# Kernel optimization log

Measured on AMD Instinct MI355X. Metric: run time of the kernel, lower is better.

The kernel has to match this reference:

```python
import jax, jax.numpy as jnp
import numpy as np


def silu(x):
    return x * jax.nn.sigmoid(x)


def conv1x1(x, w, s, b, act):
    # x: [B,Ci,H,W], w: [Co,Ci]; BN folded into per-channel scale s / bias b
    y = jnp.einsum('oi,bihw->bohw', w, x) * s[None, :, None, None] + b[None, :, None, None]
    return silu(y) if act else y


def dwconv3x3(x, w, s, b):
    # depthwise 3x3, groups=C, padding SAME (autopad=1); w: [C,1,3,3]
    y = jax.lax.conv_general_dilated(
        x, w, window_strides=(1, 1), padding=[(1, 1), (1, 1)],
        dimension_numbers=('NCHW', 'OIHW', 'NCHW'),
        feature_group_count=x.shape[1])
    return y * s[None, :, None, None] + b[None, :, None, None]


def attention(x, qkv_w, qkv_s, qkv_b, pe_w, pe_s, pe_b, proj_w, proj_s, proj_b,
              num_heads=4, key_dim=32, head_dim=64):
    B, C, H, W = x.shape
    N = H * W
    scale = key_dim ** -0.5
    qkv = conv1x1(x, qkv_w, qkv_s, qkv_b, act=False)          # [B, C+2*nh*kd, H, W]
    qkv = qkv.reshape(B, num_heads, key_dim * 2 + head_dim, N)
    q = qkv[:, :, :key_dim]                                    # [B,nh,kd,N]
    k = qkv[:, :, key_dim:2 * key_dim]                         # [B,nh,kd,N]
    v = qkv[:, :, 2 * key_dim:]                                # [B,nh,hd,N]
    attn = jnp.einsum('bhdi,bhdj->bhij', q, k) * scale         # [B,nh,N,N]
    attn = jax.nn.softmax(attn, axis=-1)
    out = jnp.einsum('bhdj,bhij->bhdi', v, attn)               # [B,nh,hd,N]
    out = out.reshape(B, C, H, W) + dwconv3x3(v.reshape(B, C, H, W), pe_w, pe_s, pe_b)
    return conv1x1(out, proj_w, proj_s, proj_b, act=False)


def setup_inputs() -> dict:
    key = jax.random.key(0)
    ks = jax.random.split(key, 32)
    B, C1, H, W = 4, 512, 48, 48
    c = C1 // 2  # 256
    h = c + 2 * 32 * 4  # 512
    d = {'x': jax.random.normal(ks[0], (B, C1, H, W), jnp.float32)}
    def w(i, shape):
        return jax.random.normal(ks[i], shape, jnp.float32) * 0.05
    def s(i, n):
        return jax.random.uniform(ks[i], (n,), jnp.float32, 0.5, 1.5)
    def b(i, n):
        return jax.random.normal(ks[i], (n,), jnp.float32) * 0.05
    d['cv1_w'], d['cv1_s'], d['cv1_b'] = w(1, (2 * c, C1)), s(2, 2 * c), b(3, 2 * c)
    d['qkv_w'], d['qkv_s'], d['qkv_b'] = w(4, (h, c)), s(5, h), b(6, h)
    d['pe_w'], d['pe_s'], d['pe_b'] = w(7, (c, 1, 3, 3)), s(8, c), b(9, c)
    d['proj_w'], d['proj_s'], d['proj_b'] = w(10, (c, c)), s(11, c), b(12, c)
    d['ffn1_w'], d['ffn1_s'], d['ffn1_b'] = w(13, (2 * c, c)), s(14, 2 * c), b(15, 2 * c)
    d['ffn2_w'], d['ffn2_s'], d['ffn2_b'] = w(16, (c, 2 * c)), s(17, c), b(18, c)
    d['cv2_w'], d['cv2_s'], d['cv2_b'] = w(19, (C1, 2 * c)), s(20, C1), b(21, C1)
    return d


def reference(x, cv1_w, cv1_s, cv1_b, qkv_w, qkv_s, qkv_b, pe_w, pe_s, pe_b,
              proj_w, proj_s, proj_b, ffn1_w, ffn1_s, ffn1_b, ffn2_w, ffn2_s, ffn2_b,
              cv2_w, cv2_s, cv2_b):
    c = cv1_w.shape[0] // 2  # hidden channels (256)
    ab = conv1x1(x, cv1_w, cv1_s, cv1_b, act=True)
    a, bb = ab[:, :c], ab[:, c:]
    bb = bb + attention(bb, qkv_w, qkv_s, qkv_b, pe_w, pe_s, pe_b,
                        proj_w, proj_s, proj_b)
    f = conv1x1(bb, ffn1_w, ffn1_s, ffn1_b, act=True)
    bb = bb + conv1x1(f, ffn2_w, ffn2_s, ffn2_b, act=False)
    return conv1x1(jnp.concatenate([a, bb], axis=1), cv2_w, cv2_s, cv2_b, act=True)
```

## Files before the change

### kernel.cpp

```cpp
#include <hip/hip_runtime.h>
#include <math.h>

#define N_SP 2304
#define HW 48

typedef unsigned short u16;
typedef short s8v  __attribute__((ext_vector_type(8)));
typedef short s4v  __attribute__((ext_vector_type(4)));
typedef u16   u16x8 __attribute__((ext_vector_type(8)));
typedef float f32x4 __attribute__((ext_vector_type(4)));
typedef unsigned u32x4 __attribute__((ext_vector_type(4)));

__device__ __forceinline__ short f2bf(float x) {
    unsigned u = __float_as_uint(x);
    u += 0x7FFFu + ((u >> 16) & 1u);
    return (short)(u >> 16);
}
__device__ __forceinline__ float bf2f(u16 u) {
    return __uint_as_float((unsigned)u << 16);
}
__device__ __forceinline__ float fexp2(float x) { return __builtin_amdgcn_exp2f(x); }
__device__ __forceinline__ float frcp(float x)  { return __builtin_amdgcn_rcpf(x); }
__device__ __forceinline__ float fsilu(float v) {
    return v * frcp(1.f + fexp2(-1.4426950408889634f * v));
}
__device__ __forceinline__ unsigned cvtpk(float lo, float hi) {
    unsigned r;
    asm("v_cvt_pk_bf16_f32 %0, %1, %2" : "=v"(r) : "v"(lo), "v"(hi));
    return r;
}
__device__ __forceinline__ void gload16(const void* g, void* l) {
    __builtin_amdgcn_global_load_lds(
        (const __attribute__((address_space(1))) void*)g,
        (__attribute__((address_space(3))) void*)l, 16, 0, 0);
}
__device__ __forceinline__ void bar_lgkm() {
    asm volatile("s_waitcnt lgkmcnt(0)" ::: "memory");
    __builtin_amdgcn_s_barrier();
}

__global__ __launch_bounds__(256) void prep(
    const float* __restrict__ X, u16* __restrict__ XT,
    const float* __restrict__ s0, const float* __restrict__ s1,
    const float* __restrict__ s2, const float* __restrict__ s3,
    const float* __restrict__ s4, const float* __restrict__ s5,
    u16* __restrict__ d0, u16* __restrict__ d1, u16* __restrict__ d2,
    u16* __restrict__ d3, u16* __restrict__ d4, u16* __restrict__ d5)
{
    __shared__ float tile[64][65];
    const int t = threadIdx.x;
    if (blockIdx.x < 960) {
        int id = blockIdx.x * 256 + t;
        const int c0 = 65536, c1 = c0 + 32768, c2 = c1 + 16384,
                  c3 = c2 + 32768, c4 = c3 + 32768, c5 = c4 + 65536;
        if (id >= c5) return;
        const float* s; u16* d; int off;
        if      (id < c0) { s = s0; d = d0; off = id; }
        else if (id < c1) { s = s1; d = d1; off = id - c0; }
        else if (id < c2) { s = s2; d = d2; off = id - c1; }
        else if (id < c3) { s = s3; d = d3; off = id - c2; }
        else if (id < c4) { s = s4; d = d4; off = id - c3; }
        else              { s = s5; d = d5; off = id - c4; }
        float4 v = ((const float4*)s)[off];
        s4v p; p[0] = f2bf(v.x); p[1] = f2bf(v.y); p[2] = f2bf(v.z); p[3] = f2bf(v.w);
        ((s4v*)d)[off] = p;
        return;
    }
    const int bid = blockIdx.x - 960;
    const int n0 = (bid % 36) * 64, c0 = ((bid / 36) & 7) * 64, b = bid / 288;
    const float* src = X + (long)b * 512 * N_SP;
    u16* dst = XT + (long)b * N_SP * 512;
    #pragma unroll
    for (int it = 0; it < 16; ++it) {
        int id = t + 256 * it;
        int cl = id >> 6, nl = id & 63;
        tile[cl][nl] = src[(long)(c0 + cl) * N_SP + n0 + nl];
    }
    __syncthreads();
    #pragma unroll
    for (int it = 0; it < 16; ++it) {
        int id = t + 256 * it;
        int nl = id >> 6, cl = id & 63;
        dst[(long)(n0 + nl) * 512 + c0 + cl] = f2bf(tile[cl][nl]);
    }
}

template <int NO, int OMODE>
__global__ __launch_bounds__(256) void mfma_gemm(
    const u16* __restrict__ A1, const u16* __restrict__ A2, int K1,
    int sA1, int sA2, int K,
    const u16* __restrict__ W,
    const float* __restrict__ S, const float* __restrict__ Bi,
    const u16* __restrict__ Res, int sR,
    void* __restrict__ OutP, u16* __restrict__ OutT, int sO, int Mtot,
    int act)
{
    __shared__ u16 Al[3][64][64];
    __shared__ u16 Bl[3][64][64];
    const int t  = threadIdx.x;
    const int p = blockIdx.x;
    const int cx = p & 7, q = p >> 3;
    const int n0 = (cx * 18 + q / NO) * 64;
    const int o0 = (q % NO) * 64;
    const int lane = t & 63, w = t >> 6;
    const int wn = (w & 1) * 32, wo = (w >> 1) * 32;
    const int li = lane & 15, g = lane >> 4;

    const int b_blk = n0 / N_SP;
    const int n_in0 = n0 - b_blk * N_SP;

    f32x4 acc[2][2];
    #pragma unroll
    for (int fm = 0; fm < 2; ++fm)
        #pragma unroll
        for (int fn = 0; fn < 2; ++fn) acc[fm][fn] = f32x4{0.f, 0.f, 0.f, 0.f};

    auto issue = [&](int buf, int k0) {
        #pragma unroll
        for (int qq = 0; qq < 2; ++qq) {
            int c = t + qq * 256;
            int row = c >> 3;
            int col = ((c & 7) ^ (row & 7)) * 8;
            int kk = k0 + col;
            const u16* ga = (kk < K1) ? (A1 + (long)(n0 + row) * sA1 + kk)
                                      : (A2 + (long)(n0 + row) * sA2 + (kk - K1));
            gload16(ga, (u16*)Al[buf] + (qq * 256 + w * 64) * 8);
            gload16(W + (long)(o0 + row) * K + k0 + col,
                    (u16*)Bl[buf] + (qq * 256 + w * 64) * 8);
        }
    };

    const int NK = K >> 6;
    issue(0, 0);
    if (NK > 1) issue(1, 64);

    for (int ks = 0; ks < NK; ++ks) {
        if (ks + 1 < NK) asm volatile("s_waitcnt vmcnt(4)" ::: "memory");
        else             asm volatile("s_waitcnt vmcnt(0)" ::: "memory");
        __builtin_amdgcn_s_barrier();
        if (ks + 2 < NK) issue((ks + 2) % 3, (ks + 2) << 6);
        const int cur = ks % 3;
        #pragma unroll
        for (int k2 = 0; k2 < 2; ++k2) {
            s8v af[2], bfv[2];
            #pragma unroll
            for (int fm = 0; fm < 2; ++fm) {
                int row = wn + fm * 16 + li;
                af[fm] = *(const s8v*)&Al[cur][row][((g + 4 * k2) ^ (li & 7)) * 8];
            }
            #pragma unroll
            for (int fn = 0; fn < 2; ++fn) {
                int row = wo + fn * 16 + li;
                bfv[fn] = *(const s8v*)&Bl[cur][row][((g + 4 * k2) ^ (li & 7)) * 8];
            }
            #pragma unroll
            for (int fm = 0; fm < 2; ++fm)
                #pragma unroll
                for (int fn = 0; fn < 2; ++fn)
                    acc[fm][fn] = __builtin_amdgcn_mfma_f32_16x16x32_bf16(
                        af[fm], bfv[fn], acc[fm][fn], 0, 0, 0);
        }
    }

    #pragma unroll
    for (int fn = 0; fn < 2; ++fn) {
        const int o = o0 + wo + fn * 16 + li;
        const float sc2 = S[o], bi = Bi[o];
        #pragma unroll
        for (int fm = 0; fm < 2; ++fm) {
            const int nb  = n0 + wn + fm * 16 + 4 * g;
            const int nib = n_in0 + wn + fm * 16 + 4 * g;
            float y[4];
            #pragma unroll
            for (int r = 0; r < 4; ++r) {
                float v = acc[fm][fn][r] * sc2 + bi;
                if (act) v = fsilu(v);
                y[r] = v;
            }
            if (Res) {
                #pragma unroll
                for (int r = 0; r < 4; ++r)
                    y[r] += bf2f(Res[(long)(nb + r) * sR + o]);
            }
            if (OMODE == 0) {
                u16* O = (u16*)OutP;
                #pragma unroll
                for (int r = 0; r < 4; ++r)
                    O[(long)(nb + r) * sO + o] = (u16)f2bf(y[r]);
            } else if (OMODE == 1 || OMODE == 3) {
                u16* O = (u16*)OutP + (long)b_blk * Mtot * N_SP + (long)o * N_SP + nib;
                s4v pk;
                #pragma unroll
                for (int r = 0; r < 4; ++r) pk[r] = f2bf(y[r]);
                *(s4v*)O = pk;
                if (OMODE == 3) {
                    #pragma unroll
                    for (int r = 0; r < 4; ++r)
                        OutT[(long)(nb + r) * 512 + o] = (u16)f2bf(y[r]);
                }
            } else {
                float* O = (float*)OutP + (long)b_blk * Mtot * N_SP + (long)o * N_SP + nib;
                *(float4*)O = make_float4(y[0], y[1], y[2], y[3]);
            }
        }
    }
}

__global__ __launch_bounds__(256) void attn_mfma(const u16* __restrict__ qkv,
    const u16* __restrict__ qkvT,
    u16* __restrict__ Opart, float* __restrict__ mpart, float* __restrict__ lpart)
{
    const int N = N_SP;
    __shared__ u16 Klds[2][64][40];
    __shared__ u16 Vlds[2][64][72];

    const int p = blockIdx.x;
    const int cx = p & 7, q = p >> 3;
    const int i0 = (q % 18) * 128;
    const int bhz = cx + 8 * (q / 18);
    const int bh = bhz & 15, z = bhz >> 4;
    const int b = bh >> 2, h = bh & 3;
    const int t = threadIdx.x;
    const int w = t >> 6;
    const int lane = t & 63;
    const int li = lane & 15;
    const int g  = lane >> 4;
    const float qscale = 0.17677669529663687f * 1.4426950408889634f;

    const u16* qp  = qkv  + ((long)b * 512 + (long)h * 128) * N;
    const u16* vp  = qp + 64L * N;
    const u16* qTp = qkvT + (long)b * N * 512 + h * 128;

    const int ia = i0 + w * 16 + li;
    const int ib = ia + 64;

    s8v qf[2];
    {
        s8v qa = *(const s8v*)(qTp + (long)ia * 512 + 8 * g);
        s8v qb = *(const s8v*)(qTp + (long)ib * 512 + 8 * g);
        #pragma unroll
        for (int r = 0; r < 8; ++r) {
            qf[0][r] = f2bf(bf2f((u16)qa[r]) * qscale);
            qf[1][r] = f2bf(bf2f((u16)qb[r]) * qscale);
        }
    }

    f32x4 oacc[2][4];
    #pragma unroll
    for (int q2 = 0; q2 < 2; ++q2)
        #pragma unroll
        for (int dt = 0; dt < 4; ++dt) oacc[q2][dt] = f32x4{0.f, 0.f, 0.f, 0.f};
    float m_run[2] = {-1e30f, -1e30f}, l_run[2] = {0.f, 0.f};

    const int kj2 = t & 63;
    const int kd  = (t >> 6) * 8;
    const int vd  = t >> 2;
    const int vjb = (t & 3) * 16;

    const int jbase = z * 576;
    u16x8 kr, vr0, vr1;
    auto ldregs = [&](int j0) {
        kr  = *(const u16x8*)(qTp + (long)(j0 + kj2) * 512 + 32 + kd);
        vr0 = *(const u16x8*)(vp + (long)vd * N + j0 + vjb);
        vr1 = *(const u16x8*)(vp + (long)vd * N + j0 + vjb + 8);
    };

    ldregs(jbase);
    *(u16x8*)&Klds[0][kj2][kd]     = kr;
    *(u16x8*)&Vlds[0][vd][vjb]     = vr0;
    *(u16x8*)&Vlds[0][vd][vjb + 8] = vr1;
    ldregs(jbase + 64);
    bar_lgkm();

    int cur = 0;
    for (int it = 0; it < 9; ++it) {
        if (it + 1 < 9) {
            *(u16x8*)&Klds[cur ^ 1][kj2][kd]     = kr;
            *(u16x8*)&Vlds[cur ^ 1][vd][vjb]     = vr0;
            *(u16x8*)&Vlds[cur ^ 1][vd][vjb + 8] = vr1;
            if (it + 2 < 9) ldregs(jbase + (it + 2) * 64);
        }

        f32x4 sacc[2][4];
        __builtin_amdgcn_s_setprio(1);
        #pragma unroll
        for (int js = 0; js < 4; ++js) {
            s8v kf = *(const s8v*)&Klds[cur][js * 16 + li][8 * g];
            f32x4 zz = f32x4{0.f, 0.f, 0.f, 0.f};
            sacc[0][js] = __builtin_amdgcn_mfma_f32_16x16x32_bf16(kf, qf[0], zz, 0, 0, 0);
            sacc[1][js] = __builtin_amdgcn_mfma_f32_16x16x32_bf16(kf, qf[1], zz, 0, 0, 0);
        }
        __builtin_amdgcn_s_setprio(0);

        #pragma unroll
        for (int q2 = 0; q2 < 2; ++q2) {
            float tm = -1e30f;
            #pragma unroll
            for (int js = 0; js < 4; ++js)
                #pragma unroll
                for (int r = 0; r < 4; ++r) tm = fmaxf(tm, sacc[q2][js][r]);
            tm = fmaxf(tm, __shfl_xor(tm, 16, 64));
            tm = fmaxf(tm, __shfl_xor(tm, 32, 64));
            if (__any(tm > m_run[q2] + 8.f)) {
                float mnew = fmaxf(m_run[q2], tm);
                float scl  = fexp2(m_run[q2] - mnew);
                l_run[q2] *= scl;
                #pragma unroll
                for (int dt = 0; dt < 4; ++dt) oacc[q2][dt] *= scl;
                m_run[q2] = mnew;
            }
            float ts = 0.f;
            #pragma unroll
            for (int js = 0; js < 4; ++js)
                #pragma unroll
                for (int r = 0; r < 4; ++r) {
                    float pv = fexp2(sacc[q2][js][r] - m_run[q2]);
                    sacc[q2][js][r] = pv;
                    ts += pv;
                }
            ts += __shfl_xor(ts, 16, 64);
            ts += __shfl_xor(ts, 32, 64);
            l_run[q2] += ts;
        }

        __builtin_amdgcn_s_setprio(1);
        #pragma unroll
        for (int ks = 0; ks < 2; ++ks) {
            s8v pf[2];
            #pragma unroll
            for (int q2 = 0; q2 < 2; ++q2) {
                u32x4 pw;
                pw[0] = cvtpk(sacc[q2][2 * ks][0],     sacc[q2][2 * ks][1]);
                pw[1] = cvtpk(sacc[q2][2 * ks][2],     sacc[q2][2 * ks][3]);
                pw[2] = cvtpk(sacc[q2][2 * ks + 1][0], sacc[q2][2 * ks + 1][1]);
                pw[3] = cvtpk(sacc[q2][2 * ks + 1][2], sacc[q2][2 * ks + 1][3]);
                pf[q2] = __builtin_bit_cast(s8v, pw);
            }
            #pragma unroll
            for (int dt = 0; dt < 4; ++dt) {
                int d = dt * 16 + li;
                s4v lo = *(const s4v*)&Vlds[cur][d][32 * ks + 4 * g];
                s4v hi = *(const s4v*)&Vlds[cur][d][32 * ks + 16 + 4 * g];
                s8v vf = __builtin_shufflevector(lo, hi, 0, 1, 2, 3, 4, 5, 6, 7);
                oacc[0][dt] = __builtin_amdgcn_mfma_f32_16x16x32_bf16(vf, pf[0], oacc[0][dt], 0, 0, 0);
                oacc[1][dt] = __builtin_amdgcn_mfma_f32_16x16x32_bf16(vf, pf[1], oacc[1][dt], 0, 0, 0);
            }
        }
        __builtin_amdgcn_s_setprio(0);

        if (it + 1 < 9) bar_lgkm();
        cur ^= 1;
    }

    const long cb = (long)(z * 16 + bh);
    #pragma unroll
    for (int q2 = 0; q2 < 2; ++q2) {
        const int i = q2 ? ib : ia;
        #pragma unroll
        for (int dt = 0; dt < 4; ++dt)
            #pragma unroll
            for (int r = 0; r < 4; ++r)
                Opart[(cb * 64 + dt * 16 + 4 * g + r) * N + i] = (u16)f2bf(oacc[q2][dt][r]);
        if (g == 0) {
            mpart[cb * N + i] = m_run[q2];
            lpart[cb * N + i] = l_run[q2];
        }
    }
}

__global__ __launch_bounds__(256) void attn_combine(
    const u16* __restrict__ Opart, const float* __restrict__ mpart,
    const float* __restrict__ lpart, const u16* __restrict__ qkv,
    const float* __restrict__ pw, const float* __restrict__ ps,
    const float* __restrict__ pb, u16* __restrict__ attnT)
{
    const int N = N_SP;
    const int i0 = blockIdx.x * 64;
    const int bh = blockIdx.y;
    const int b = bh >> 2, h = bh & 3;
    const int t = threadIdx.x;
    const int il = t & 63, dq = t >> 6;
    const int d0 = dq * 16;
    const int i = i0 + il;

    float mm[4], ll[4];
    #pragma unroll
    for (int c = 0; c < 4; ++c) {
        mm[c] = mpart[((long)(c * 16 + bh)) * N + i];
        ll[c] = lpart[((long)(c * 16 + bh)) * N + i];
    }
    float ms = fmaxf(fmaxf(mm[0], mm[1]), fmaxf(mm[2], mm[3]));
    float wc[4], lsum = 0.f;
    #pragma unroll
    for (int c = 0; c < 4; ++c) {
        wc[c] = fexp2(mm[c] - ms);
        lsum += wc[c] * ll[c];
    }
    float inv = frcp(lsum);

    const int y = i / HW, x = i - (i / HW) * HW;
    const int y0ok = (y > 0), y1ok = (y < HW - 1);
    const int x0ok = (x > 0), x1ok = (x < HW - 1);
    const u16* vbase = qkv + ((long)b * 512 + (long)h * 128 + 64) * N;

    u16 ob[16];
    #pragma unroll
    for (int dd = 0; dd < 16; ++dd) {
        const int d = d0 + dd;
        const int cg = h * 64 + d;
        float o = 0.f;
        #pragma unroll
        for (int c = 0; c < 4; ++c)
            o += wc[c] * bf2f(Opart[((long)(c * 16 + bh) * 64 + d) * N + i]);
        o *= inv;
        const u16* src = vbase + (long)d * N;
        const float* w9 = pw + cg * 9;
        float s = 0.f;
        #pragma unroll
        for (int dy = -1; dy <= 1; ++dy) {
            if ((dy < 0 && !y0ok) || (dy > 0 && !y1ok)) continue;
            const u16* row = src + (y + dy) * HW;
            if (x0ok) s += w9[(dy + 1) * 3 + 0] * bf2f(row[x - 1]);
            s += w9[(dy + 1) * 3 + 1] * bf2f(row[x]);
            if (x1ok) s += w9[(dy + 1) * 3 + 2] * bf2f(row[x + 1]);
        }
        o += s * ps[cg] + pb[cg];
        ob[dd] = (u16)f2bf(o);
    }
    u16* dst = attnT + ((long)b * N + i) * 256 + h * 64 + d0;
    *(u16x8*)dst       = *(u16x8*)&ob[0];
    *(u16x8*)(dst + 8) = *(u16x8*)&ob[8];
}

extern "C" void kernel_launch(void* const* d_in, const int* in_sizes, int n_in,
                              void* d_out, int out_size, void* d_ws, size_t ws_size,
                              hipStream_t stream)
{
    const long N = N_SP;
    const float* x      = (const float*)d_in[0];
    const float* cv1_w  = (const float*)d_in[1];
    const float* cv1_s  = (const float*)d_in[2];
    const float* cv1_b  = (const float*)d_in[3];
    const float* qkv_w  = (const float*)d_in[4];
    const float* qkv_s  = (const float*)d_in[5];
    const float* qkv_b  = (const float*)d_in[6];
    const float* pe_w   = (const float*)d_in[7];
    const float* pe_s   = (const float*)d_in[8];
    const float* pe_b   = (const float*)d_in[9];
    const float* proj_w = (const float*)d_in[10];
    const float* proj_s = (const float*)d_in[11];
    const float* proj_b = (const float*)d_in[12];
    const float* ffn1_w = (const float*)d_in[13];
    const float* ffn1_s = (const float*)d_in[14];
    const float* ffn1_b = (const float*)d_in[15];
    const float* ffn2_w = (const float*)d_in[16];
    const float* ffn2_s = (const float*)d_in[17];
    const float* ffn2_b = (const float*)d_in[18];
    const float* cv2_w  = (const float*)d_in[19];
    const float* cv2_s  = (const float*)d_in[20];
    const float* cv2_b  = (const float*)d_in[21];
    float* out = (float*)d_out;

    u16* ws = (u16*)d_ws;
    u16* xT      = ws;
    u16* abT     = xT      + 4L * N * 512;
    u16* qkvb    = abT     + 4L * N * 512;
    u16* qkvT    = qkvb    + 4L * N * 512;
    u16* attnT   = qkvT    + 4L * N * 512;
    u16* bb2T    = attnT   + 4L * N * 256;
    u16* fT      = bb2T    + 4L * N * 256;
    u16* bb3T    = fT      + 4L * N * 512;
    u16* w_cv1   = bb3T    + 4L * N * 256;
    u16* w_qkv   = w_cv1   + 512L * 512;
    u16* w_proj  = w_qkv   + 512L * 256;
    u16* w_ffn1  = w_proj  + 256L * 256;
    u16* w_ffn2  = w_ffn1  + 512L * 256;
    u16* w_cv2   = w_ffn2  + 256L * 512;
    u16* Opart   = w_cv2   + 512L * 512;
    float* mpart = (float*)(Opart + 4L * 16 * 64 * N);
    float* lpart = mpart + 4L * 16 * N;

    dim3 blk(256);
    const int BIGK = 1 << 28;

    prep<<<2112, blk, 0, stream>>>(x, xT,
        cv1_w, qkv_w, proj_w, ffn1_w, ffn2_w, cv2_w,
        w_cv1, w_qkv, w_proj, w_ffn1, w_ffn2, w_cv2);

    mfma_gemm<8, 0><<<1152, blk, 0, stream>>>(
        xT, nullptr, BIGK, 512, 0, 512, w_cv1, cv1_s, cv1_b,
        nullptr, 0, abT, nullptr, 512, 512, 1);

    mfma_gemm<8, 3><<<1152, blk, 0, stream>>>(
        abT + 256, nullptr, BIGK, 512, 0, 256, w_qkv, qkv_s, qkv_b,
        nullptr, 0, qkvb, qkvT, 0, 512, 0);

    attn_mfma<<<1152, blk, 0, stream>>>(qkvb, qkvT, Opart, mpart, lpart);

    attn_combine<<<dim3(36, 16), blk, 0, stream>>>(
        Opart, mpart, lpart, qkvb, pe_w, pe_s, pe_b, attnT);

    mfma_gemm<4, 0><<<576, blk, 0, stream>>>(
        attnT, nullptr, BIGK, 256, 0, 256, w_proj, proj_s, proj_b,
        abT + 256, 512, bb2T, nullptr, 256, 256, 0);

    mfma_gemm<8, 0><<<1152, blk, 0, stream>>>(
        bb2T, nullptr, BIGK, 256, 0, 256, w_ffn1, ffn1_s, ffn1_b,
        nullptr, 0, fT, nullptr, 512, 512, 1);

    mfma_gemm<4, 0><<<576, blk, 0, stream>>>(
        fT, nullptr, BIGK, 512, 0, 512, w_ffn2, ffn2_s, ffn2_b,
        bb2T, 256, bb3T, nullptr, 256, 256, 0);

    mfma_gemm<8, 2><<<1152, blk, 0, stream>>>(
        abT, bb3T, 256, 512, 256, 512, w_cv2, cv2_s, cv2_b,
        nullptr, 0, out, nullptr, 0, 512, 1);
}
```

Measured before the change: 146.5 us.

## Load K/V straight from global in attention and transpose partial-output layout

The flash-attention kernel no longer stages K and V tiles through double-buffered LDS with barriers. Each wave now reads its MFMA fragments directly from global memory and relies on cache reuse across waves. The PV MFMA operand order is swapped so the accumulators hold query rows, which means the online-softmax rescale factors are fetched per row with lane shuffles. Opart is stored as [chunk][N][64] so the combine kernel can read it with contiguous 16-byte vector loads. The risk is unhidden global-load latency and repeated fetches of the same K/V data by all four waves, with no prefetching.

```diff
diff --git a/kernel.cpp b/kernel.cpp
--- a/kernel.cpp
+++ b/kernel.cpp
@@ -33,10 +33,6 @@
     __builtin_amdgcn_global_load_lds(
         (const __attribute__((address_space(1))) void*)g,
         (__attribute__((address_space(3))) void*)l, 16, 0, 0);
-}
-__device__ __forceinline__ void bar_lgkm() {
-    asm volatile("s_waitcnt lgkmcnt(0)" ::: "memory");
-    __builtin_amdgcn_s_barrier();
 }
 
 __global__ __launch_bounds__(256) void prep(
@@ -211,9 +207,6 @@
     u16* __restrict__ Opart, float* __restrict__ mpart, float* __restrict__ lpart)
 {
     const int N = N_SP;
-    __shared__ u16 Klds[2][64][40];
-    __shared__ u16 Vlds[2][64][72];
-
     const int p = blockIdx.x;
     const int cx = p & 7, q = p >> 3;
     const int i0 = (q % 18) * 128;
@@ -222,22 +215,20 @@
     const int b = bh >> 2, h = bh & 3;
     const int t = threadIdx.x;
     const int w = t >> 6;
-    const int lane = t & 63;
-    const int li = lane & 15;
-    const int g  = lane >> 4;
+    const int li = t & 15;
+    const int g  = (t & 63) >> 4;
     const float qscale = 0.17677669529663687f * 1.4426950408889634f;
 
-    const u16* qp  = qkv  + ((long)b * 512 + (long)h * 128) * N;
-    const u16* vp  = qp + 64L * N;
+    const u16* vp  = qkv  + ((long)b * 512 + (long)h * 128 + 64) * N;
     const u16* qTp = qkvT + (long)b * N * 512 + h * 128;
 
-    const int ia = i0 + w * 16 + li;
+    const int ia = i0 + w * 16;
     const int ib = ia + 64;
 
     s8v qf[2];
     {
-        s8v qa = *(const s8v*)(qTp + (long)ia * 512 + 8 * g);
-        s8v qb = *(const s8v*)(qTp + (long)ib * 512 + 8 * g);
+        s8v qa = *(const s8v*)(qTp + (long)(ia + li) * 512 + 8 * g);
+        s8v qb = *(const s8v*)(qTp + (long)(ib + li) * 512 + 8 * g);
         #pragma unroll
         for (int r = 0; r < 8; ++r) {
             qf[0][r] = f2bf(bf2f((u16)qa[r]) * qscale);
@@ -252,45 +243,30 @@
         for (int dt = 0; dt < 4; ++dt) oacc[q2][dt] = f32x4{0.f, 0.f, 0.f, 0.f};
     float m_run[2] = {-1e30f, -1e30f}, l_run[2] = {0.f, 0.f};
 
-    const int kj2 = t & 63;
-    const int kd  = (t >> 6) * 8;
-    const int vd  = t >> 2;
-    const int vjb = (t & 3) * 16;
-
     const int jbase = z * 576;
-    u16x8 kr, vr0, vr1;
-    auto ldregs = [&](int j0) {
-        kr  = *(const u16x8*)(qTp + (long)(j0 + kj2) * 512 + 32 + kd);
-        vr0 = *(const u16x8*)(vp + (long)vd * N + j0 + vjb);
-        vr1 = *(const u16x8*)(vp + (long)vd * N + j0 + vjb + 8);
-    };
-
-    ldregs(jbase);
-    *(u16x8*)&Klds[0][kj2][kd]     = kr;
-    *(u16x8*)&Vlds[0][vd][vjb]     = vr0;
-    *(u16x8*)&Vlds[0][vd][vjb + 8] = vr1;
-    ldregs(jbase + 64);
-    bar_lgkm();
-
-    int cur = 0;
     for (int it = 0; it < 9; ++it) {
-        if (it + 1 < 9) {
-            *(u16x8*)&Klds[cur ^ 1][kj2][kd]     = kr;
-            *(u16x8*)&Vlds[cur ^ 1][vd][vjb]     = vr0;
-            *(u16x8*)&Vlds[cur ^ 1][vd][vjb + 8] = vr1;
-            if (it + 2 < 9) ldregs(jbase + (it + 2) * 64);
-        }
+        const int j0 = jbase + it * 64;
 
         f32x4 sacc[2][4];
         __builtin_amdgcn_s_setprio(1);
         #pragma unroll
         for (int js = 0; js < 4; ++js) {
-            s8v kf = *(const s8v*)&Klds[cur][js * 16 + li][8 * g];
+            s8v kf = *(const s8v*)(qTp + (long)(j0 + js * 16 + li) * 512 + 32 + 8 * g);
             f32x4 zz = f32x4{0.f, 0.f, 0.f, 0.f};
             sacc[0][js] = __builtin_amdgcn_mfma_f32_16x16x32_bf16(kf, qf[0], zz, 0, 0, 0);
             sacc[1][js] = __builtin_amdgcn_mfma_f32_16x16x32_bf16(kf, qf[1], zz, 0, 0, 0);
         }
         __builtin_amdgcn_s_setprio(0);
+
+        s4v vlo[2][4], vhi[2][4];
+        #pragma unroll
+        for (int ks = 0; ks < 2; ++ks)
+            #pragma unroll
+            for (int dt = 0; dt < 4; ++dt) {
+                const u16* vb = vp + (long)(dt * 16 + li) * N + j0 + 32 * ks + 4 * g;
+                vlo[ks][dt] = *(const s4v*)vb;
+                vhi[ks][dt] = *(const s4v*)(vb + 16);
+            }
 
         #pragma unroll
         for (int q2 = 0; q2 < 2; ++q2) {
@@ -305,9 +281,18 @@
                 float mnew = fmaxf(m_run[q2], tm);
                 float scl  = fexp2(m_run[q2] - mnew);
                 l_run[q2] *= scl;
-                #pragma unroll
-                for (int dt = 0; dt < 4; ++dt) oacc[q2][dt] *= scl;
                 m_run[q2] = mnew;
+                float s0 = __shfl(scl, 4 * g + 0, 16);
+                float s1 = __shfl(scl, 4 * g + 1, 16);
+                float s2 = __shfl(scl, 4 * g + 2, 16);
+                float s3 = __shfl(scl, 4 * g + 3, 16);
+                #pragma unroll
+                for (int dt = 0; dt < 4; ++dt) {
+                    oacc[q2][dt][0] *= s0;
+                    oacc[q2][dt][1] *= s1;
+                    oacc[q2][dt][2] *= s2;
+                    oacc[q2][dt][3] *= s3;
+                }
             }
             float ts = 0.f;
             #pragma unroll
@@ -338,32 +323,28 @@
             }
             #pragma unroll
             for (int dt = 0; dt < 4; ++dt) {
-                int d = dt * 16 + li;
-                s4v lo = *(const s4v*)&Vlds[cur][d][32 * ks + 4 * g];
-                s4v hi = *(const s4v*)&Vlds[cur][d][32 * ks + 16 + 4 * g];
-                s8v vf = __builtin_shufflevector(lo, hi, 0, 1, 2, 3, 4, 5, 6, 7);
-                oacc[0][dt] = __builtin_amdgcn_mfma_f32_16x16x32_bf16(vf, pf[0], oacc[0][dt], 0, 0, 0);
-                oacc[1][dt] = __builtin_amdgcn_mfma_f32_16x16x32_bf16(vf, pf[1], oacc[1][dt], 0, 0, 0);
+                s8v vf = __builtin_shufflevector(vlo[ks][dt], vhi[ks][dt],
+                                                 0, 1, 2, 3, 4, 5, 6, 7);
+                oacc[0][dt] = __builtin_amdgcn_mfma_f32_16x16x32_bf16(pf[0], vf, oacc[0][dt], 0, 0, 0);
+                oacc[1][dt] = __builtin_amdgcn_mfma_f32_16x16x32_bf16(pf[1], vf, oacc[1][dt], 0, 0, 0);
             }
         }
         __builtin_amdgcn_s_setprio(0);
-
-        if (it + 1 < 9) bar_lgkm();
-        cur ^= 1;
     }
 
     const long cb = (long)(z * 16 + bh);
     #pragma unroll
     for (int q2 = 0; q2 < 2; ++q2) {
-        const int i = q2 ? ib : ia;
+        const int ibq = q2 ? ib : ia;
         #pragma unroll
         for (int dt = 0; dt < 4; ++dt)
             #pragma unroll
             for (int r = 0; r < 4; ++r)
-                Opart[(cb * 64 + dt * 16 + 4 * g + r) * N + i] = (u16)f2bf(oacc[q2][dt][r]);
+                Opart[(cb * N + ibq + 4 * g + r) * 64 + dt * 16 + li] =
+                    (u16)f2bf(oacc[q2][dt][r]);
         if (g == 0) {
-            mpart[cb * N + i] = m_run[q2];
-            lpart[cb * N + i] = l_run[q2];
+            mpart[cb * N + ibq + li] = m_run[q2];
+            lpart[cb * N + ibq + li] = l_run[q2];
         }
     }
 }
@@ -398,6 +379,21 @@
     }
     float inv = frcp(lsum);
 
+    float acc16[16];
+    #pragma unroll
+    for (int dd = 0; dd < 16; ++dd) acc16[dd] = 0.f;
+    #pragma unroll
+    for (int c = 0; c < 4; ++c) {
+        const u16* op = Opart + ((long)(c * 16 + bh) * N + i) * 64 + d0;
+        u16x8 v0 = *(const u16x8*)op;
+        u16x8 v1 = *(const u16x8*)(op + 8);
+        #pragma unroll
+        for (int dd = 0; dd < 8; ++dd) {
+            acc16[dd]     += wc[c] * bf2f((u16)v0[dd]);
+            acc16[8 + dd] += wc[c] * bf2f((u16)v1[dd]);
+        }
+    }
+
     const int y = i / HW, x = i - (i / HW) * HW;
     const int y0ok = (y > 0), y1ok = (y < HW - 1);
     const int x0ok = (x > 0), x1ok = (x < HW - 1);
@@ -408,11 +404,7 @@
     for (int dd = 0; dd < 16; ++dd) {
         const int d = d0 + dd;
         const int cg = h * 64 + d;
-        float o = 0.f;
-        #pragma unroll
-        for (int c = 0; c < 4; ++c)
-            o += wc[c] * bf2f(Opart[((long)(c * 16 + bh) * 64 + d) * N + i]);
-        o *= inv;
+        float o = acc16[dd] * inv;
         const u16* src = vbase + (long)d * N;
         const float* w9 = pw + cg * 9;
         float s = 0.f;
```

Measured after the change: 222.8 us. 1.52x slower.
